# Performance work log

Hardware: AMD Instinct MI355X
Metric: run time of the kernel (lower is better)

The kernel has to match this reference:

```python
import jax, jax.numpy as jnp
import numpy as np
from jax import lax

L, E, H, V, B, S = 25, 64, 8, 30000, 1000, 512


def setup_inputs() -> dict:
    key = jax.random.key(0)
    ks = jax.random.split(key, 24)
    p = lambda k, shape: (jax.random.normal(k, shape) * 0.1).astype(jnp.float32)
    inp = {
        "x": jax.random.randint(ks[0], (B, S), 0, V),
        "embedding": p(ks[1], (V, E)),
        # layer 0 (input dim = E)
        "W_xz0": p(ks[2], (E, H)), "W_hz0": p(ks[3], (H, H)), "b_z0": p(ks[4], (H,)),
        "W_xr0": p(ks[5], (E, H)), "W_hr0": p(ks[6], (H, H)), "b_r0": p(ks[7], (H,)),
        "W_xH0": p(ks[8], (E, H)), "W_rH0": p(ks[9], (H, H)), "b_H0": p(ks[10], (H,)),
        # layers 1..L-1 stacked (input dim = H)
        "W_xz": p(ks[11], (L - 1, H, H)), "W_hz": p(ks[12], (L - 1, H, H)), "b_z": p(ks[13], (L - 1, H)),
        "W_xr": p(ks[14], (L - 1, H, H)), "W_hr": p(ks[15], (L - 1, H, H)), "b_r": p(ks[16], (L - 1, H)),
        "W_xH": p(ks[17], (L - 1, H, H)), "W_rH": p(ks[18], (L - 1, H, H)), "b_H": p(ks[19], (L - 1, H)),
        "W_hy": p(ks[20], (H, 1)), "b_y": p(ks[21], (1,)),
    }
    return inp


def _cell(x_t, h, Wxz, Whz, bz, Wxr, Whr, br, WxH, WrH, bH):
    z = jax.nn.sigmoid(x_t @ Wxz + h @ Whz + bz)
    r = jax.nn.sigmoid(x_t @ Wxr + h @ Whr + br)
    Hc = jnp.tanh(x_t @ WxH + (h * r) @ WrH + bH)
    return h * (1.0 - z) + z * Hc


def reference(x, embedding, W_xz0, W_hz0, b_z0, W_xr0, W_hr0, b_r0, W_xH0, W_rH0, b_H0,
              W_xz, W_hz, b_z, W_xr, W_hr, b_r, W_xH, W_rH, b_H, W_hy, b_y):
    emb = embedding[x]                     # [B, S, E]
    bsz = x.shape[0]
    h0 = jnp.zeros((L, bsz, H), dtype=embedding.dtype)

    def time_step(h_all, x_t):            # h_all: [L, B, H]; x_t: [B, E]
        h_new0 = _cell(x_t, h_all[0], W_xz0, W_hz0, b_z0, W_xr0, W_hr0, b_r0, W_xH0, W_rH0, b_H0)

        def layer_step(inp_t, ws):
            Wxz, Whz, bz, Wxr, Whr, br, WxH, WrH, bH, h_prev = ws
            h_new = _cell(inp_t, h_prev, Wxz, Whz, bz, Wxr, Whr, br, WxH, WrH, bH)
            return h_new, h_new

        _, h_rest = lax.scan(layer_step, h_new0,
                             (W_xz, W_hz, b_z, W_xr, W_hr, b_r, W_xH, W_rH, b_H, h_all[1:]))
        return jnp.concatenate([h_new0[None], h_rest], axis=0), None

    h_last, _ = lax.scan(time_step, h0, jnp.swapaxes(emb, 0, 1))  # scan over S
    logits = h_last[-1] @ W_hy + b_y       # [B, 1]
    return logits.squeeze(-1), h_last
```

## Files before the change

kernel.cpp:

```cpp
#include <hip/hip_runtime.h>
#include <hip/hip_bf16.h>
#include <stdint.h>

#define L_ 25
#define E_ 64
#define H_ 8
#define B_ 1000
#define S_ 512
#define GQ 4
#define NCELL (L_ * GQ)
#define TPBR (NCELL * 8)
#define NSUPER (S_ / 2 + L_ - 1)
#define HS 12
#define XG 20

typedef float v2f __attribute__((ext_vector_type(2)));
typedef float v4f __attribute__((ext_vector_type(4)));

#define PIN(x) asm volatile("" : "+v"(x))

__device__ __forceinline__ v2f pkfma(v2f a, v2f b, v2f c) {
  v2f d;
  asm("v_pk_fma_f32 %0, %1, %2, %3" : "=v"(d) : "v"(a), "v"(b), "v"(c));
  return d;
}
__device__ __forceinline__ v2f pkfma_l(v2f a, v2f b, v2f c) {
  v2f d;
  asm("v_pk_fma_f32 %0, %1, %2, %3 op_sel:[0,0,0] op_sel_hi:[0,1,1]"
      : "=v"(d) : "v"(a), "v"(b), "v"(c));
  return d;
}
__device__ __forceinline__ v2f pkfma_h(v2f a, v2f b, v2f c) {
  v2f d;
  asm("v_pk_fma_f32 %0, %1, %2, %3 op_sel:[1,0,0] op_sel_hi:[1,1,1]"
      : "=v"(d) : "v"(a), "v"(b), "v"(c));
  return d;
}
__device__ __forceinline__ v2f pkadd(v2f a, v2f b) {
  v2f d;
  asm("v_pk_add_f32 %0, %1, %2" : "=v"(d) : "v"(a), "v"(b));
  return d;
}
__device__ __forceinline__ v2f vlo(v4f v) { return __builtin_shufflevector(v, v, 0, 1); }
__device__ __forceinline__ v2f vhi(v4f v) { return __builtin_shufflevector(v, v, 2, 3); }
__device__ __forceinline__ v2f mk2(float a, float b) { v2f r; r.x = a; r.y = b; return r; }

#define CHAIN8(acc, ma, mb, w)            \
  acc = pkfma_l(vlo(ma), w[0], acc);      \
  acc = pkfma_h(vlo(ma), w[1], acc);      \
  acc = pkfma_l(vhi(ma), w[2], acc);      \
  acc = pkfma_h(vhi(ma), w[3], acc);      \
  acc = pkfma_l(vlo(mb), w[4], acc);      \
  acc = pkfma_h(vlo(mb), w[5], acc);      \
  acc = pkfma_l(vhi(mb), w[6], acc);      \
  acc = pkfma_h(vhi(mb), w[7], acc);

#define CHAIN4P(acc, ma, mb, w)           \
  acc = pkfma(vlo(ma), w[0], acc);        \
  acc = pkfma(vhi(ma), w[1], acc);        \
  acc = pkfma(vlo(mb), w[2], acc);        \
  acc = pkfma(vhi(mb), w[3], acc);

__device__ __forceinline__ float ulo(uint32_t u) { return __uint_as_float(u << 16); }
__device__ __forceinline__ float uhi(uint32_t u) { return __uint_as_float(u & 0xffff0000u); }

__device__ __forceinline__ float toF(float v) { return v; }
__device__ __forceinline__ float toF(__hip_bfloat16 v) { return __bfloat162float(v); }
__device__ __forceinline__ void stP(float* p, float v) { *p = v; }
__device__ __forceinline__ void stP(__hip_bfloat16* p, float v) { *p = __float2bfloat16(v); }

__device__ __forceinline__ v2f loadC2(const float* p) { return *(const v2f*)p; }
__device__ __forceinline__ v2f loadC2(const __hip_bfloat16* p) {
  const uint32_t u = *(const uint32_t*)p;
  return mk2(ulo(u), uhi(u));
}

__device__ __forceinline__ void load8f(const __hip_bfloat16* p, float* o) {
  const uint4 v = *(const uint4*)p;
  o[0] = ulo(v.x); o[1] = uhi(v.x); o[2] = ulo(v.y); o[3] = uhi(v.y);
  o[4] = ulo(v.z); o[5] = uhi(v.z); o[6] = ulo(v.w); o[7] = uhi(v.w);
}
__device__ __forceinline__ void load8f(const float* p, float* o) {
  const float4 a = ((const float4*)p)[0];
  const float4 b = ((const float4*)p)[1];
  o[0] = a.x; o[1] = a.y; o[2] = a.z; o[3] = a.w;
  o[4] = b.x; o[5] = b.y; o[6] = b.z; o[7] = b.w;
}

__device__ __forceinline__ void st4(float* p, float a, float b, float c, float d) {
  float4 v; v.x = a; v.y = b; v.z = c; v.w = d;
  *(float4*)p = v;
}
__device__ __forceinline__ void st4(__hip_bfloat16* p, float a, float b, float c, float d) {
  __hip_bfloat16 t[4] = {__float2bfloat16(a), __float2bfloat16(b),
                         __float2bfloat16(c), __float2bfloat16(d)};
  *(ushort4*)p = *(ushort4*)t;
}

__device__ __forceinline__ float sigmo(float x) {
  return __builtin_amdgcn_rcpf(1.f + __expf(-x));
}
__device__ __forceinline__ float tanh_(float x) {
  const float e = __expf(-2.f * x);
  return fmaf(2.f, __builtin_amdgcn_rcpf(1.f + e), -1.f);
}

__device__ __forceinline__ void detect64(const unsigned short* __restrict__ u,
                                         int tid, float* fl) {
  if (tid < 64) {
    float m = 0.f;
#pragma unroll
    for (int k = 0; k < 4; ++k) {
      const uint32_t q = u[tid * 4 + k];
      float v = fabsf(__uint_as_float(q << 16));
      if (!(v < 1e30f)) v = 1e30f;
      m = fmaxf(m, v);
    }
#pragma unroll
    for (int off = 32; off; off >>= 1) m = fmaxf(m, __shfl_down(m, off, 64));
    if (tid == 0) *fl = (m > 2.0f) ? 0.f : 1.f;
  }
}

template <typename T, typename PT>
__device__ __forceinline__ void pre_body(
    const int* __restrict__ x, const void* __restrict__ embv,
    const void* __restrict__ Wzv, const void* __restrict__ Wrv,
    const void* __restrict__ Whv, PT* __restrict__ pre,
    float* WL, float* TBb) {
  const T* emb = (const T*)embv;
  const T* Wz = (const T*)Wzv;
  const T* Wr = (const T*)Wrv;
  const T* Wh = (const T*)Whv;
  const int tid = threadIdx.x;

  for (int idx = tid; idx < 64 * 24; idx += 256) {
    const int k = idx / 24, c = idx - k * 24;
    float w;
    if (c < 16) w = toF(((c & 1) ? Wr : Wz)[k * 8 + (c >> 1)]);
    else        w = toF(Wh[k * 8 + (c - 16)]);
    WL[idx] = w;
  }
  __syncthreads();

  const int tok = blockIdx.x * 256 + tid;
  const int t = x[tok];

  v2f acc[12];
#pragma unroll
  for (int q = 0; q < 12; ++q) acc[q] = mk2(0.f, 0.f);

  for (int kb = 0; kb < 8; ++kb) {
    float e[8];
    load8f(emb + (size_t)t * E_ + kb * 8, e);
#pragma unroll
    for (int k8 = 0; k8 < 8; ++k8) {
      const v4f* wr = (const v4f*)(WL + (kb * 8 + k8) * 24);
      const v2f ee = mk2(e[k8], e[k8]);
#pragma unroll
      for (int q = 0; q < 6; ++q) {
        const v4f w4 = wr[q];
        acc[2 * q]     = pkfma(ee, vlo(w4), acc[2 * q]);
        acc[2 * q + 1] = pkfma(ee, vhi(w4), acc[2 * q + 1]);
      }
    }
  }

  const int wid = tid >> 6, lane = tid & 63;
  float* tb = TBb + wid * (24 * 65);
#pragma unroll
  for (int q = 0; q < 12; ++q) {
    tb[(2 * q) * 65 + lane] = acc[q].x;
    tb[(2 * q + 1) * 65 + lane] = acc[q].y;
  }
  asm volatile("s_waitcnt lgkmcnt(0)" ::: "memory");
  __builtin_amdgcn_wave_barrier();

  PT* ob = pre + (size_t)(blockIdx.x * 256 + wid * 64) * 24;
#pragma unroll
  for (int it = 0; it < 6; ++it) {
    const int F0 = it * 256 + lane * 4;
    float o[4];
#pragma unroll
    for (int e2 = 0; e2 < 4; ++e2) {
      const int F = F0 + e2;
      const int tk = F / 24;
      const int c = F - tk * 24;
      o[e2] = tb[c * 65 + tk];
    }
    st4(ob + F0, o[0], o[1], o[2], o[3]);
  }
}

template <typename PT>
__global__ __launch_bounds__(256, 4) void gru_pre(
    const int* __restrict__ x, const void* __restrict__ emb,
    const void* __restrict__ Wz, const void* __restrict__ Wr,
    const void* __restrict__ Wh, PT* __restrict__ pre) {
  __shared__ __align__(16) float WL[64 * 24];
  __shared__ __align__(16) float TB[4][24 * 65];
  __shared__ float fl;
  detect64((const unsigned short*)emb, threadIdx.x, &fl);
  __syncthreads();
  if (fl != 0.f) pre_body<__hip_bfloat16, PT>(x, emb, Wz, Wr, Wh, pre, WL, &TB[0][0]);
  else           pre_body<float, PT>(x, emb, Wz, Wr, Wh, pre, WL, &TB[0][0]);
}

template <typename T, typename PT>
__device__ __forceinline__ void rec_body(
    const PT* __restrict__ pre,
    const void* __restrict__ Whz0v, const void* __restrict__ bz0v,
    const void* __restrict__ Whr0v, const void* __restrict__ br0v,
    const void* __restrict__ WrH0v, const void* __restrict__ bH0v,
    const void* __restrict__ Wxzv, const void* __restrict__ Whzv,
    const void* __restrict__ bzv, const void* __restrict__ Wxrv,
    const void* __restrict__ Whrv, const void* __restrict__ brv,
    const void* __restrict__ WxHv, const void* __restrict__ WrHv,
    const void* __restrict__ bHv, const void* __restrict__ Whyv,
    const void* __restrict__ byv, void* __restrict__ outv,
    float* hsh, float* hrsh, float* xbuf) {
  const T* Whz0 = (const T*)Whz0v; const T* bz0 = (const T*)bz0v;
  const T* Whr0 = (const T*)Whr0v; const T* br0 = (const T*)br0v;
  const T* WrH0 = (const T*)WrH0v; const T* bH0 = (const T*)bH0v;
  const T* Wxz = (const T*)Wxzv;   const T* Whz = (const T*)Whzv;
  const T* bz = (const T*)bzv;     const T* Wxr = (const T*)Wxrv;
  const T* Whr = (const T*)Whrv;   const T* br = (const T*)brv;
  const T* WxH = (const T*)WxHv;   const T* WrH = (const T*)WrHv;
  const T* bH = (const T*)bHv;     const T* Why = (const T*)Whyv;
  const T* by = (const T*)byv;     T* out = (T*)outv;

  const int tid = threadIdx.x;
  const int gi = tid >> 3;
  const int j = tid & 7;
  const int l = gi >> 2;
  const int g = gi & 3;
  const int b = blockIdx.x * GQ + g;

  for (int i = tid; i < NCELL * HS; i += TPBR) { hsh[i] = 0.f; hrsh[i] = 0.f; }
  for (int i = tid; i < 2 * NCELL * XG; i += TPBR) xbuf[i] = 0.f;

  v2f wzrx[8], wzrh[8], wxh2[4], wrh2[4], bzr;
  float vbh;
  if (l == 0) {
#pragma unroll
    for (int k = 0; k < 8; ++k) {
      wzrh[k] = mk2(toF(Whz0[k * 8 + j]), toF(Whr0[k * 8 + j]));
      wzrx[k] = mk2(0.f, 0.f);
    }
#pragma unroll
    for (int q = 0; q < 4; ++q) {
      wrh2[q] = mk2(toF(WrH0[(2 * q) * 8 + j]), toF(WrH0[(2 * q + 1) * 8 + j]));
      wxh2[q] = mk2(0.f, 0.f);
    }
    bzr = mk2(toF(bz0[j]), toF(br0[j]));
    vbh = toF(bH0[j]);
  } else {
    const int base = (l - 1) * 64;
#pragma unroll
    for (int k = 0; k < 8; ++k) {
      wzrx[k] = mk2(toF(Wxz[base + k * 8 + j]), toF(Wxr[base + k * 8 + j]));
      wzrh[k] = mk2(toF(Whz[base + k * 8 + j]), toF(Whr[base + k * 8 + j]));
    }
#pragma unroll
    for (int q = 0; q < 4; ++q) {
      wxh2[q] = mk2(toF(WxH[base + (2 * q) * 8 + j]), toF(WxH[base + (2 * q + 1) * 8 + j]));
      wrh2[q] = mk2(toF(WrH[base + (2 * q) * 8 + j]), toF(WrH[base + (2 * q + 1) * 8 + j]));
    }
    bzr = mk2(toF(bz[(l - 1) * 8 + j]), toF(br[(l - 1) * 8 + j]));
    vbh = toF(bH[(l - 1) * 8 + j]);
  }
#pragma unroll
  for (int k = 0; k < 8; ++k) { PIN(wzrx[k]); PIN(wzrh[k]); }
#pragma unroll
  for (int q = 0; q < 4; ++q) { PIN(wxh2[q]); PIN(wrh2[q]); }
  PIN(bzr); PIN(vbh);

  const PT* ppr = pre + (size_t)b * (S_ * 24);
  v2f czrA = mk2(0.f, 0.f), czrB = mk2(0.f, 0.f);
  float chA = 0.f, chB = 0.f;
  if (l == 0) {
    czrA = loadC2(ppr + 2 * j);      chA = toF(ppr[16 + j]);
    czrB = loadC2(ppr + 24 + 2 * j); chB = toF(ppr[24 + 16 + j]);
  }

  float* hgw = hsh + gi * HS;
  float* hrg = hrsh + gi * HS;
  float* hgwj = hgw + j;
  float* hrgj = hrg + j;
  const int gp = (gi >= GQ) ? (gi - GQ) * XG : 0;
  const float* xpe = xbuf + NCELL * XG + gp;
  const float* xpo = xbuf + gp;
  float* xce = xbuf + gi * XG;
  float* xco = xbuf + NCELL * XG + gi * XG;

  float hown = 0.f;

  __syncthreads();

  for (int s = 0; s < NSUPER; ++s) {
    const unsigned rel = (unsigned)(s - l);
    if (rel < (unsigned)(S_ / 2)) {
      const float* xp = (s & 1) ? xpo : xpe;
      float* xc = (s & 1) ? xco : xce;

      const v4f h01 = ((const v4f*)hgw)[0];
      const v4f h23 = ((const v4f*)hgw)[1];
      const v4f xa0 = ((const v4f*)xp)[0];
      const v4f xb0 = ((const v4f*)xp)[1];
      const v4f xa1 = ((const v4f*)xp)[2];
      const v4f xb1 = ((const v4f*)xp)[3];

      v2f nzrA = mk2(0.f, 0.f), nzrB = mk2(0.f, 0.f);
      float nhA = 0.f, nhB = 0.f;
      const bool pf = (l == 0) && (rel + 1u < (unsigned)(S_ / 2));
      if (pf) {
        const PT* pn = ppr + (2 * rel + 2) * 24;
        nzrA = loadC2(pn + 2 * j);      nhA = toF(pn[16 + j]);
        nzrB = loadC2(pn + 24 + 2 * j); nhB = toF(pn[24 + 16 + j]);
      }

      v2f azrh = bzr;
      CHAIN8(azrh, h01, h23, wzrh);
      v2f azrxA = czrA;
      CHAIN8(azrxA, xa0, xb0, wzrx);
      v2f ahA = mk2(chA, vbh);
      CHAIN4P(ahA, xa0, xb0, wxh2);
      v2f azrxB = czrB;
      CHAIN8(azrxB, xa1, xb1, wzrx);
      v2f ahB = mk2(chB, vbh);
      CHAIN4P(ahB, xa1, xb1, wxh2);

      const v2f azrA = pkadd(azrh, azrxA);
      const float rA = sigmo(azrA.y);
      *hrgj = hown * rA;
      __builtin_amdgcn_wave_barrier();

      const v4f r01 = ((const v4f*)hrg)[0];
      const v4f r23 = ((const v4f*)hrg)[1];
      const float zA = sigmo(azrA.x);
      CHAIN4P(ahA, r01, r23, wrh2);
      const float hcA = tanh_(ahA.x + ahA.y);
      const float hn0 = fmaf(zA, hcA - hown, hown);
      *hgwj = hn0;
      xc[j] = hn0;
      __builtin_amdgcn_wave_barrier();

      const v4f g01 = ((const v4f*)hgw)[0];
      const v4f g23 = ((const v4f*)hgw)[1];
      v2f azrhB = bzr;
      CHAIN8(azrhB, g01, g23, wzrh);
      const v2f azrB = pkadd(azrhB, azrxB);
      const float rB = sigmo(azrB.y);
      *hrgj = hn0 * rB;
      __builtin_amdgcn_wave_barrier();

      const v4f q01 = ((const v4f*)hrg)[0];
      const v4f q23 = ((const v4f*)hrg)[1];
      const float zB = sigmo(azrB.x);
      CHAIN4P(ahB, q01, q23, wrh2);
      const float hcB = tanh_(ahB.x + ahB.y);
      const float hn1 = fmaf(zB, hcB - hn0, hn0);
      *hgwj = hn1;
      xc[8 + j] = hn1;
      hown = hn1;
      czrA = nzrA; chA = nhA; czrB = nzrB; chB = nhB;
    }
    __syncthreads();
  }

  stP(out + B_ + (l * B_ + b) * H_ + j, hown);
  if (l == L_ - 1 && j == 0) {
    float ssum = toF(by[0]);
#pragma unroll
    for (int k = 0; k < 8; ++k) ssum = fmaf(hgw[k], toF(Why[k]), ssum);
    stP(out + b, ssum);
  }
}

template <typename PT>
__global__ __launch_bounds__(TPBR, 4) void gru_rec(
    const void* __restrict__ emb, const PT* __restrict__ pre,
    const void* __restrict__ Whz0, const void* __restrict__ bz0,
    const void* __restrict__ Whr0, const void* __restrict__ br0,
    const void* __restrict__ WrH0, const void* __restrict__ bH0,
    const void* __restrict__ Wxz, const void* __restrict__ Whz,
    const void* __restrict__ bz, const void* __restrict__ Wxr,
    const void* __restrict__ Whr, const void* __restrict__ br,
    const void* __restrict__ WxH, const void* __restrict__ WrH,
    const void* __restrict__ bH, const void* __restrict__ Why,
    const void* __restrict__ by, void* __restrict__ out) {
  __shared__ __align__(16) float hsh[NCELL * HS];
  __shared__ __align__(16) float hrsh[NCELL * HS];
  __shared__ __align__(16) float xbuf[2 * NCELL * XG];
  __shared__ float fl;
  detect64((const unsigned short*)emb, threadIdx.x, &fl);
  __syncthreads();
  if (fl != 0.f)
    rec_body<__hip_bfloat16, PT>(pre, Whz0, bz0, Whr0, br0, WrH0, bH0, Wxz, Whz,
                                 bz, Wxr, Whr, br, WxH, WrH, bH, Why, by, out,
                                 hsh, hrsh, xbuf);
  else
    rec_body<float, PT>(pre, Whz0, bz0, Whr0, br0, WrH0, bH0, Wxz, Whz, bz, Wxr,
                        Whr, br, WxH, WrH, bH, Why, by, out, hsh, hrsh, xbuf);
}

template <typename PT>
static void launch_all(void* const* d_in, PT* pre, void* d_out, hipStream_t stream) {
  gru_pre<PT><<<B_ * S_ / 256, 256, 0, stream>>>(
      (const int*)d_in[0], d_in[1], d_in[2], d_in[5], d_in[8], pre);
  gru_rec<PT><<<B_ / GQ, TPBR, 0, stream>>>(
      d_in[1], pre, d_in[3], d_in[4], d_in[6], d_in[7], d_in[9], d_in[10],
      d_in[11], d_in[12], d_in[13], d_in[14], d_in[15], d_in[16], d_in[17],
      d_in[18], d_in[19], d_in[20], d_in[21], d_out);
}

extern "C" void kernel_launch(void* const* d_in, const int* in_sizes, int n_in,
                              void* d_out, int out_size, void* d_ws, size_t ws_size,
                              hipStream_t stream) {
  const size_t needF = (size_t)B_ * S_ * 24 * sizeof(float);
  if (ws_size >= needF)
    launch_all<float>(d_in, (float*)d_ws, d_out, stream);
  else
    launch_all<__hip_bfloat16>(d_in, (__hip_bfloat16*)d_ws, d_out, stream);
}
```

Baseline: 408.7 us.

## Process four timesteps per superstep and fuse GRU gate nonlinearities

The wavefront schedule now advances four timesteps per block-wide superstep instead of two. This halves the number of __syncthreads barriers and halves the pipeline-fill overhead relative to the per-layer work. The per-step gate math is rewritten so that the z-sigmoid, the tanh and the final blend share a single reciprocal, with the exponentials clamped. In exchange, each superstep holds more registers for the prefetched layer-0 inputs, the exchange buffer grows (XG 20→36), and the merged formula may change rounding slightly.

```diff
diff --git a/kernel.cpp b/kernel.cpp
--- a/kernel.cpp
+++ b/kernel.cpp
@@ -10,9 +10,10 @@
 #define GQ 4
 #define NCELL (L_ * GQ)
 #define TPBR (NCELL * 8)
-#define NSUPER (S_ / 2 + L_ - 1)
+#define TS 4
+#define NSUPER (S_ / TS + L_ - 1)
 #define HS 12
-#define XG 20
+#define XG 36
 
 typedef float v2f __attribute__((ext_vector_type(2)));
 typedef float v4f __attribute__((ext_vector_type(4)));
@@ -99,10 +100,6 @@
 
 __device__ __forceinline__ float sigmo(float x) {
   return __builtin_amdgcn_rcpf(1.f + __expf(-x));
-}
-__device__ __forceinline__ float tanh_(float x) {
-  const float e = __expf(-2.f * x);
-  return fmaf(2.f, __builtin_amdgcn_rcpf(1.f + e), -1.f);
 }
 
 __device__ __forceinline__ void detect64(const unsigned short* __restrict__ u,
@@ -205,6 +202,31 @@
   if (fl != 0.f) pre_body<__hip_bfloat16, PT>(x, emb, Wz, Wr, Wh, pre, WL, &TB[0][0]);
   else           pre_body<float, PT>(x, emb, Wz, Wr, Wh, pre, WL, &TB[0][0]);
 }
+
+#define TIMESTEP(hprev, axK, ahK, slot, hnout)                       \
+  {                                                                  \
+    const v4f h01_ = ((const v4f*)hgw)[0];                           \
+    const v4f h23_ = ((const v4f*)hgw)[1];                           \
+    v2f azrh_ = bzr;                                                 \
+    CHAIN8(azrh_, h01_, h23_, wzrh);                                 \
+    const v2f azr_ = pkadd(azrh_, axK);                              \
+    const float r_ = sigmo(azr_.y);                                  \
+    *hrgj = (hprev) * r_;                                            \
+    __builtin_amdgcn_wave_barrier();                                 \
+    const v4f r01_ = ((const v4f*)hrg)[0];                           \
+    const v4f r23_ = ((const v4f*)hrg)[1];                           \
+    CHAIN4P(ahK, r01_, r23_, wrh2);                                  \
+    const float ah_ = ahK.x + ahK.y;                                 \
+    const float ez_ = __expf(fminf(-azr_.x, 30.f));                  \
+    const float eh_ = __expf(fminf(-2.f * ah_, 30.f));               \
+    const float t_ = (hprev) * ez_;                                  \
+    const float num_ = fmaf(eh_, t_ - 1.f, t_ + 1.f);                \
+    const float den_ = (1.f + ez_) * (1.f + eh_);                    \
+    hnout = num_ * __builtin_amdgcn_rcpf(den_);                      \
+    *hgwj = hnout;                                                   \
+    xc[(slot) * 8 + j] = hnout;                                      \
+    __builtin_amdgcn_wave_barrier();                                 \
+  }
 
 template <typename T, typename PT>
 __device__ __forceinline__ void rec_body(
@@ -276,11 +298,13 @@
   PIN(bzr); PIN(vbh);
 
   const PT* ppr = pre + (size_t)b * (S_ * 24);
-  v2f czrA = mk2(0.f, 0.f), czrB = mk2(0.f, 0.f);
-  float chA = 0.f, chB = 0.f;
+  v2f czr0 = mk2(0.f, 0.f), czr1 = czr0, czr2 = czr0, czr3 = czr0;
+  float ch0 = 0.f, ch1 = 0.f, ch2 = 0.f, ch3 = 0.f;
   if (l == 0) {
-    czrA = loadC2(ppr + 2 * j);      chA = toF(ppr[16 + j]);
-    czrB = loadC2(ppr + 24 + 2 * j); chB = toF(ppr[24 + 16 + j]);
+    czr0 = loadC2(ppr + 0 * 24 + 2 * j);  ch0 = toF(ppr[0 * 24 + 16 + j]);
+    czr1 = loadC2(ppr + 1 * 24 + 2 * j);  ch1 = toF(ppr[1 * 24 + 16 + j]);
+    czr2 = loadC2(ppr + 2 * 24 + 2 * j);  ch2 = toF(ppr[2 * 24 + 16 + j]);
+    czr3 = loadC2(ppr + 3 * 24 + 2 * j);  ch3 = toF(ppr[3 * 24 + 16 + j]);
   }
 
   float* hgw = hsh + gi * HS;
@@ -299,71 +323,50 @@
 
   for (int s = 0; s < NSUPER; ++s) {
     const unsigned rel = (unsigned)(s - l);
-    if (rel < (unsigned)(S_ / 2)) {
+    if (rel < (unsigned)(S_ / TS)) {
       const float* xp = (s & 1) ? xpo : xpe;
       float* xc = (s & 1) ? xco : xce;
 
-      const v4f h01 = ((const v4f*)hgw)[0];
-      const v4f h23 = ((const v4f*)hgw)[1];
       const v4f xa0 = ((const v4f*)xp)[0];
       const v4f xb0 = ((const v4f*)xp)[1];
       const v4f xa1 = ((const v4f*)xp)[2];
       const v4f xb1 = ((const v4f*)xp)[3];
 
-      v2f nzrA = mk2(0.f, 0.f), nzrB = mk2(0.f, 0.f);
-      float nhA = 0.f, nhB = 0.f;
-      const bool pf = (l == 0) && (rel + 1u < (unsigned)(S_ / 2));
+      v2f nzr0 = mk2(0.f, 0.f), nzr1 = nzr0, nzr2 = nzr0, nzr3 = nzr0;
+      float nh0 = 0.f, nh1 = 0.f, nh2 = 0.f, nh3 = 0.f;
+      const bool pf = (l == 0) && (rel + 1u < (unsigned)(S_ / TS));
       if (pf) {
-        const PT* pn = ppr + (2 * rel + 2) * 24;
-        nzrA = loadC2(pn + 2 * j);      nhA = toF(pn[16 + j]);
-        nzrB = loadC2(pn + 24 + 2 * j); nhB = toF(pn[24 + 16 + j]);
+        const PT* pn = ppr + (TS * rel + 4) * 24;
+        nzr0 = loadC2(pn + 0 * 24 + 2 * j);  nh0 = toF(pn[0 * 24 + 16 + j]);
+        nzr1 = loadC2(pn + 1 * 24 + 2 * j);  nh1 = toF(pn[1 * 24 + 16 + j]);
+        nzr2 = loadC2(pn + 2 * 24 + 2 * j);  nh2 = toF(pn[2 * 24 + 16 + j]);
+        nzr3 = loadC2(pn + 3 * 24 + 2 * j);  nh3 = toF(pn[3 * 24 + 16 + j]);
       }
 
-      v2f azrh = bzr;
-      CHAIN8(azrh, h01, h23, wzrh);
-      v2f azrxA = czrA;
-      CHAIN8(azrxA, xa0, xb0, wzrx);
-      v2f ahA = mk2(chA, vbh);
-      CHAIN4P(ahA, xa0, xb0, wxh2);
-      v2f azrxB = czrB;
-      CHAIN8(azrxB, xa1, xb1, wzrx);
-      v2f ahB = mk2(chB, vbh);
-      CHAIN4P(ahB, xa1, xb1, wxh2);
-
-      const v2f azrA = pkadd(azrh, azrxA);
-      const float rA = sigmo(azrA.y);
-      *hrgj = hown * rA;
-      __builtin_amdgcn_wave_barrier();
-
-      const v4f r01 = ((const v4f*)hrg)[0];
-      const v4f r23 = ((const v4f*)hrg)[1];
-      const float zA = sigmo(azrA.x);
-      CHAIN4P(ahA, r01, r23, wrh2);
-      const float hcA = tanh_(ahA.x + ahA.y);
-      const float hn0 = fmaf(zA, hcA - hown, hown);
-      *hgwj = hn0;
-      xc[j] = hn0;
-      __builtin_amdgcn_wave_barrier();
-
-      const v4f g01 = ((const v4f*)hgw)[0];
-      const v4f g23 = ((const v4f*)hgw)[1];
-      v2f azrhB = bzr;
-      CHAIN8(azrhB, g01, g23, wzrh);
-      const v2f azrB = pkadd(azrhB, azrxB);
-      const float rB = sigmo(azrB.y);
-      *hrgj = hn0 * rB;
-      __builtin_amdgcn_wave_barrier();
-
-      const v4f q01 = ((const v4f*)hrg)[0];
-      const v4f q23 = ((const v4f*)hrg)[1];
-      const float zB = sigmo(azrB.x);
-      CHAIN4P(ahB, q01, q23, wrh2);
-      const float hcB = tanh_(ahB.x + ahB.y);
-      const float hn1 = fmaf(zB, hcB - hn0, hn0);
-      *hgwj = hn1;
-      xc[8 + j] = hn1;
-      hown = hn1;
-      czrA = nzrA; chA = nhA; czrB = nzrB; chB = nhB;
+      v2f ax0 = czr0; CHAIN8(ax0, xa0, xb0, wzrx);
+      v2f ah0 = mk2(ch0, vbh); CHAIN4P(ah0, xa0, xb0, wxh2);
+      v2f ax1 = czr1; CHAIN8(ax1, xa1, xb1, wzrx);
+      v2f ah1 = mk2(ch1, vbh); CHAIN4P(ah1, xa1, xb1, wxh2);
+
+      float hn0, hn1, hn2, hn3;
+      TIMESTEP(hown, ax0, ah0, 0, hn0);
+
+      const v4f xa2 = ((const v4f*)xp)[4];
+      const v4f xb2 = ((const v4f*)xp)[5];
+      const v4f xa3 = ((const v4f*)xp)[6];
+      const v4f xb3 = ((const v4f*)xp)[7];
+      v2f ax2 = czr2; CHAIN8(ax2, xa2, xb2, wzrx);
+      v2f ah2 = mk2(ch2, vbh); CHAIN4P(ah2, xa2, xb2, wxh2);
+      v2f ax3 = czr3; CHAIN8(ax3, xa3, xb3, wzrx);
+      v2f ah3 = mk2(ch3, vbh); CHAIN4P(ah3, xa3, xb3, wxh2);
+
+      TIMESTEP(hn0, ax1, ah1, 1, hn1);
+      TIMESTEP(hn1, ax2, ah2, 2, hn2);
+      TIMESTEP(hn2, ax3, ah3, 3, hn3);
+
+      hown = hn3;
+      czr0 = nzr0; ch0 = nh0; czr1 = nzr1; ch1 = nh1;
+      czr2 = nzr2; ch2 = nh2; czr3 = nzr3; ch3 = nh3;
     }
     __syncthreads();
   }
```

After: 395.8 us. -3.2%, faster.
